# Kernel optimization log

Measured on AMD Instinct MI355X. Metric: run time of the kernel, lower is better.

Reference implementation:

```python
import jax, jax.numpy as jnp
import numpy as np
from jax import lax

KS = 3
PAD = 1
N = KS * KS


def setup_inputs() -> dict:
    key = jax.random.key(0)
    k1, k2, k3, k4, k5, k6 = jax.random.split(key, 6)
    b, cin, cout, h, w = 4, 64, 64, 256, 256
    x = jax.random.normal(k1, (b, cin, h, w), jnp.float32)
    # offset-predicting conv: 2*N output channels, 3x3, pad 1
    p_conv_w = 0.1 * jax.random.normal(k2, (2 * N, cin, KS, KS), jnp.float32)
    p_conv_b = jnp.zeros((2 * N,), jnp.float32)
    # main conv applied to the k*k-expanded sampled map (no bias in original)
    conv_w = jax.random.normal(k3, (cout, cin, KS, KS), jnp.float32) / np.sqrt(cin * N)
    bn_gamma = 1.0 + 0.1 * jax.random.normal(k4, (cout,), jnp.float32)
    bn_beta = 0.1 * jax.random.normal(k5, (cout,), jnp.float32)
    return {"x": x, "p_conv_w": p_conv_w, "p_conv_b": p_conv_b,
            "conv_w": conv_w, "bn_gamma": bn_gamma, "bn_beta": bn_beta}


def _deform_conv(x, p_conv_w, p_conv_b, conv_w, bn_gamma, bn_beta):
    b, c, h, w = x.shape
    # offsets: (b, 2N, h, w) -> (b, h, w, 2N)
    offset = lax.conv_general_dilated(x, p_conv_w, (1, 1), ((PAD, PAD), (PAD, PAD)))
    offset = offset + p_conv_b[None, :, None, None]
    offset = jnp.transpose(offset, (0, 2, 3, 1))
    # zero-pad input; sampling coordinates live on the padded grid
    x_pad = jnp.pad(x, ((0, 0), (0, 0), (PAD, PAD), (PAD, PAD)))
    Hp, Wp = h + 2 * PAD, w + 2 * PAD
    # p = p_0 + p_n + offset  (x/y coords each of shape (b,h,w,N))
    r = jnp.arange(-(KS - 1) // 2, KS // 2 + 1, dtype=jnp.float32)  # [-1,0,1]
    pn_x, pn_y = jnp.meshgrid(r, r, indexing="ij")
    pn_x, pn_y = pn_x.reshape(-1), pn_y.reshape(-1)  # (N,)
    p0_x = jnp.arange(1, h + 1, dtype=jnp.float32)[:, None, None]  # (h,1,1)
    p0_y = jnp.arange(1, w + 1, dtype=jnp.float32)[None, :, None]  # (1,w,1)
    p_x = offset[..., :N] + p0_x + pn_x  # (b,h,w,N)
    p_y = offset[..., N:] + p0_y + pn_y
    # integer corner coords (detached / non-differentiable), clamped
    fx = jnp.floor(lax.stop_gradient(p_x))
    fy = jnp.floor(lax.stop_gradient(p_y))
    q_lt_x = jnp.clip(fx, 0, Hp - 1).astype(jnp.int32)
    q_lt_y = jnp.clip(fy, 0, Wp - 1).astype(jnp.int32)
    q_rb_x = jnp.clip(fx + 1, 0, Hp - 1).astype(jnp.int32)
    q_rb_y = jnp.clip(fy + 1, 0, Wp - 1).astype(jnp.int32)
    # clamped continuous coords (gradient flows to offsets)
    px = jnp.clip(p_x, 0, Hp - 1)
    py = jnp.clip(p_y, 0, Wp - 1)
    # bilinear weights
    ltx = q_lt_x.astype(px.dtype); lty = q_lt_y.astype(px.dtype)
    rbx = q_rb_x.astype(px.dtype); rby = q_rb_y.astype(px.dtype)
    g_lt = (1 + (ltx - px)) * (1 + (lty - py))
    g_rb = (1 - (rbx - px)) * (1 - (rby - py))
    g_lb = (1 + (ltx - px)) * (1 - (rby - py))
    g_rt = (1 - (rbx - px)) * (1 + (lty - py))
    x_flat = x_pad.reshape(b, c, Hp * Wp)

    def gather(qx, qy):
        idx = (qx * Wp + qy).reshape(b, 1, -1)  # (b,1,h*w*N)
        out = jnp.take_along_axis(x_flat, idx, axis=2)
        return out.reshape(b, c, h, w, N)

    x_off = (g_lt[:, None] * gather(q_lt_x, q_lt_y)
             + g_rb[:, None] * gather(q_rb_x, q_rb_y)
             + g_lb[:, None] * gather(q_lt_x, q_rb_y)
             + g_rt[:, None] * gather(q_rb_x, q_lt_y))  # (b,c,h,w,N)
    # conv (kernel=KS, stride=KS on k*k-expanded map) == contraction over (c,N)
    out = jnp.einsum("bchwn,ocn->bohw", x_off, conv_w.reshape(conv_w.shape[0], c, N))
    # BatchNorm2d (training-mode batch statistics) + LeakyReLU(0.1)
    mean = out.mean(axis=(0, 2, 3), keepdims=True)
    var = out.var(axis=(0, 2, 3), keepdims=True)
    y = (out - mean) * lax.rsqrt(var + 1e-5)
    y = y * bn_gamma[None, :, None, None] + bn_beta[None, :, None, None]
    return jnp.where(y > 0, y, 0.1 * y)


def reference(x, p_conv_w, p_conv_b, conv_w, bn_gamma, bn_beta):
    return _deform_conv(x, p_conv_w, p_conv_b, conv_w, bn_gamma, bn_beta)
```

## Files before the change

kernel.cpp:

```cpp
#include <hip/hip_runtime.h>
#include <math.h>

#define BB 4
#define CC 64
#define OCC 64
#define HH 256
#define WW 256
#define HP 258
#define WP 258
#define NPIX (BB * HH * WW)
#define CNT_F 262144.0f

typedef __attribute__((ext_vector_type(8))) __bf16 bf16x8;
typedef __attribute__((ext_vector_type(4))) float f32x4;

__device__ __forceinline__ float blo(unsigned u) {
    return __builtin_bit_cast(float, u << 16);
}
__device__ __forceinline__ float bhi(unsigned u) {
    return __builtin_bit_cast(float, u & 0xffff0000u);
}

__global__ __launch_bounds__(256) void pad_transpose(const float* __restrict__ x,
                                                     __bf16* __restrict__ xt) {
    int blk = blockIdx.x;
    int xchunk = blk & 3;
    int y = (blk >> 2) & 255;
    int b = blk >> 10;
    int tid = threadIdx.x;
    __shared__ float tile[64][65];
    int x0 = xchunk * 64;
    int col = tid & 63;
    int crow = tid >> 6;
    const float* xp = x + ((size_t)b * CC) * HH * WW + (size_t)y * WW + x0;
#pragma unroll
    for (int i = 0; i < 16; ++i) {
        int c = crow + i * 4;
        tile[c][col] = xp[(size_t)c * HH * WW + col];
    }
    __syncthreads();
    __bf16* op = xt + (((size_t)b * HP + (y + 1)) * WP + (x0 + 1)) * CC;
#pragma unroll
    for (int i = 0; i < 16; ++i) {
        int xl = crow + i * 4;
        op[(size_t)xl * CC + col] = (__bf16)tile[col][xl];
    }
}

__global__ void zero_border(__bf16* __restrict__ xt) {
    int i = blockIdx.x * 256 + threadIdx.x;
    const int total = BB * 1028 * CC;
    if (i >= total) return;
    int c = i & 63;
    int p = (i >> 6) % 1028;
    int b = (i >> 6) / 1028;
    int yp, xp;
    if (p < 258)      { yp = 0;           xp = p; }
    else if (p < 516) { yp = 257;         xp = p - 258; }
    else if (p < 772) { yp = p - 516 + 1; xp = 0; }
    else              { yp = p - 772 + 1; xp = 257; }
    xt[(((size_t)b * HP + yp) * WP + xp) * CC + c] = (__bf16)0.0f;
}

__global__ void reorder_weights(const float* __restrict__ cw,
                                const float* __restrict__ pw,
                                __bf16* __restrict__ wtb,
                                __bf16* __restrict__ pwb) {
    int i = blockIdx.x * 256 + threadIdx.x;
    if (i < 36864) {
        int c = i & 63;
        int n = (i >> 6) % 9;
        int oc = i / 576;
        wtb[i] = (__bf16)cw[((size_t)oc * CC + c) * 9 + n];
    } else {
        int j = i - 36864;
        if (j >= 18432) return;
        int c = j & 63;
        int n = (j >> 6) % 9;
        int oc = j / 576;
        pwb[j] = (__bf16)(oc < 18 ? pw[((size_t)oc * CC + c) * 9 + n] : 0.0f);
    }
}

__global__ __launch_bounds__(256, 8) void deform_fused(const __bf16* __restrict__ xt,
                                                       const __bf16* __restrict__ pwb,
                                                       const float* __restrict__ pb,
                                                       const __bf16* __restrict__ wtb,
                                                       float* __restrict__ out) {
    int phys = blockIdx.x;
    int blk = (phys & 7) * 2048 + (phys >> 3);
    int xh = blk & 15;
    int y  = (blk >> 4) & 255;
    int b  = blk >> 12;
    int x0 = xh * 16;
    int tid = threadIdx.x;
    int wave = tid >> 6, lane = tid & 63;
    int chp = lane & 31, half = lane >> 5;

    __shared__ __attribute__((aligned(16))) char smem[19584];
    __bf16 (*sS)[18][72] = (__bf16 (*)[18][72])smem;
    char* sAb = smem;
    float* offbuf = (float*)(smem + 18432);

    {
        const char* base = (const char*)xt + (size_t)b * HP * WP * CC * 2;
        for (int t = tid; t < 1728; t += 256) {
            int pos = t >> 5, cp = t & 31;
            int r = pos / 18, j = pos - r * 18;
            unsigned d = *(const unsigned*)(base
                + (size_t)((y + r) * WP + (x0 + j)) * (CC * 2) + cp * 4);
            *(unsigned*)&sS[r][j][cp * 2] = d;
        }
    }
    __syncthreads();

    if (wave < 2) {
        int nh = wave;
        int m = lane & 15, q = lane >> 4;
        f32x4 acc = {0.0f, 0.0f, 0.0f, 0.0f};
        const __bf16* bp = pwb + (size_t)(nh * 16 + m) * 576 + q * 8;
#pragma unroll
        for (int n = 0; n < 9; ++n) {
            int dy = n / 3, dx = n - dy * 3;
            const __bf16* abase = &sS[dy][m + dx][q * 8];
#pragma unroll
            for (int h = 0; h < 2; ++h) {
                bf16x8 a  = *(const bf16x8*)(abase + h * 32);
                bf16x8 bv = *(const bf16x8*)(bp + n * 64 + h * 32);
                acc = __builtin_amdgcn_mfma_f32_16x16x32_bf16(a, bv, acc, 0, 0, 0);
            }
        }
        int oc = nh * 16 + m;
        if (oc < 18) {
            float bias = pb[oc];
#pragma unroll
            for (int r = 0; r < 4; ++r)
                offbuf[(q * 4 + r) * 18 + oc] = acc[r] + bias;
        }
    }
    __syncthreads();

    float g0 = 0.0f, g1 = 0.0f, g2 = 0.0f, g3 = 0.0f;
    int c0 = 0, c1 = 0, c2 = 0, c3 = 0;
    if (lane < 36) {
        int t = wave * 36 + lane;
        int n = t >> 4, p = t & 15;
        float offx = offbuf[p * 18 + n];
        float offy = offbuf[p * 18 + n + 9];
        float px = offx + (float)(y + 1) + (float)(n / 3 - 1);
        float py = offy + (float)(x0 + p + 1) + (float)(n % 3 - 1);
        float fx = floorf(px), fy = floorf(py);
        float pxc = fminf(fmaxf(px, 0.0f), 257.0f);
        float pyc = fminf(fmaxf(py, 0.0f), 257.0f);
        int ltx = (int)fminf(fmaxf(fx, 0.0f), 257.0f);
        int lty = (int)fminf(fmaxf(fy, 0.0f), 257.0f);
        int rbx = (int)fminf(fmaxf(fx + 1.0f, 0.0f), 257.0f);
        int rby = (int)fminf(fmaxf(fy + 1.0f, 0.0f), 257.0f);
        float dxl = 1.0f + ((float)ltx - pxc);
        float dxr = 1.0f - ((float)rbx - pxc);
        float dyl = 1.0f + ((float)lty - pyc);
        float dyr = 1.0f - ((float)rby - pyc);
        g0 = dxl * dyl;
        g1 = dxr * dyr;
        g2 = dxl * dyr;
        g3 = dxr * dyl;
        c0 = ((ltx * WP + lty) * CC) * 2;
        c1 = ((rbx * WP + rby) * CC) * 2;
        c2 = ((ltx * WP + rby) * CC) * 2;
        c3 = ((rbx * WP + lty) * CC) * 2;
    }

    {
        const char* xbl = (const char*)xt + (size_t)b * HP * WP * CC * 2 + (size_t)chp * 4;
#pragma unroll 3
        for (int r = 0; r < 18; ++r) {
            int src = r * 2 + half;
            float gx = __shfl(g0, src, 64);
            float gy = __shfl(g1, src, 64);
            float gz = __shfl(g2, src, 64);
            float gw = __shfl(g3, src, 64);
            int vx = __shfl(c0, src, 64);
            int vy = __shfl(c1, src, 64);
            int vz = __shfl(c2, src, 64);
            int vw = __shfl(c3, src, 64);
            unsigned d0 = *(const unsigned*)(xbl + vx);
            unsigned d1 = *(const unsigned*)(xbl + vy);
            unsigned d2 = *(const unsigned*)(xbl + vz);
            unsigned d3 = *(const unsigned*)(xbl + vw);
            float lo = gx * blo(d0) + gy * blo(d1) + gz * blo(d2) + gw * blo(d3);
            float hi = gx * bhi(d0) + gy * bhi(d1) + gz * bhi(d2) + gw * bhi(d3);
            __bf16 rlo = (__bf16)lo, rhi = (__bf16)hi;
            ushort2 rv;
            rv.x = __builtin_bit_cast(unsigned short, rlo);
            rv.y = __builtin_bit_cast(unsigned short, rhi);
            int t = wave * 36 + src;
            int n = t >> 4, p = t & 15;
            unsigned bo = (unsigned)p * 1152u + (unsigned)n * 128u + (unsigned)chp * 4u;
            bo ^= (unsigned)((p & 7) << 4);
            *(ushort2*)(sAb + bo) = rv;
        }
    }
    __syncthreads();

    int m = lane & 15, q = lane >> 4;
    f32x4 acc = {0.0f, 0.0f, 0.0f, 0.0f};
    {
        unsigned rowb = (unsigned)m * 1152u;
        unsigned key = (unsigned)((m & 7) << 4);
        const __bf16* bp = wtb + (size_t)(wave * 16 + m) * 576 + q * 8;
        __builtin_amdgcn_s_setprio(1);
#pragma unroll
        for (int k0 = 0; k0 < 576; k0 += 32) {
            unsigned bo = rowb + (((unsigned)(k0 * 2 + q * 16)) ^ key);
            bf16x8 a  = *(const bf16x8*)(sAb + bo);
            bf16x8 bv = *(const bf16x8*)(bp + k0);
            acc = __builtin_amdgcn_mfma_f32_16x16x32_bf16(a, bv, acc, 0, 0, 0);
        }
        __builtin_amdgcn_s_setprio(0);
    }

    int oc = wave * 16 + m;
    float* ob = out + (((size_t)b * OCC + oc) * HH + y) * WW + x0 + q * 4;
    float4 v;
    v.x = acc[0]; v.y = acc[1]; v.z = acc[2]; v.w = acc[3];
    *(float4*)ob = v;
}

__global__ __launch_bounds__(256) void stats_kernel(const float* __restrict__ out,
                                                    float* __restrict__ stats) {
    int blk = blockIdx.x;
    int b = blk & 3;
    int oc = blk >> 2;
    const float* p = out + ((size_t)b * OCC + oc) * HH * WW;
    float s = 0.0f, q = 0.0f;
    for (int i = threadIdx.x; i < HH * WW; i += 256) {
        float v = p[i];
        s += v;
        q += v * v;
    }
#pragma unroll
    for (int d = 1; d < 64; d <<= 1) {
        s += __shfl_xor(s, d, 64);
        q += __shfl_xor(q, d, 64);
    }
    __shared__ float sm[8];
    int wave = threadIdx.x >> 6, lane = threadIdx.x & 63;
    if (lane == 0) { sm[wave] = s; sm[4 + wave] = q; }
    __syncthreads();
    if (threadIdx.x == 0) {
        float ts = sm[0] + sm[1] + sm[2] + sm[3];
        float tq = sm[4] + sm[5] + sm[6] + sm[7];
        atomicAdd(&stats[oc], ts);
        atomicAdd(&stats[64 + oc], tq);
    }
}

__global__ __launch_bounds__(256) void bn_leaky(float* __restrict__ out,
                                                const float* __restrict__ stats,
                                                const float* __restrict__ gamma,
                                                const float* __restrict__ beta) {
    int i = blockIdx.x * 256 + threadIdx.x;
    int oc = (i >> 14) & 63;
    float mean = stats[oc] * (1.0f / CNT_F);
    float var = stats[64 + oc] * (1.0f / CNT_F) - mean * mean;
    float scale = gamma[oc] * rsqrtf(var + 1e-5f);
    float shift = beta[oc] - mean * scale;
    float4* o4 = (float4*)out;
    float4 v = o4[i];
    v.x = v.x * scale + shift; v.x = v.x > 0.0f ? v.x : 0.1f * v.x;
    v.y = v.y * scale + shift; v.y = v.y > 0.0f ? v.y : 0.1f * v.y;
    v.z = v.z * scale + shift; v.z = v.z > 0.0f ? v.z : 0.1f * v.z;
    v.w = v.w * scale + shift; v.w = v.w > 0.0f ? v.w : 0.1f * v.w;
    o4[i] = v;
}

extern "C" void kernel_launch(void* const* d_in, const int* in_sizes, int n_in,
                              void* d_out, int out_size, void* d_ws, size_t ws_size,
                              hipStream_t stream) {
    (void)in_sizes; (void)n_in; (void)out_size; (void)ws_size;
    const float* x     = (const float*)d_in[0];
    const float* pw    = (const float*)d_in[1];
    const float* pb    = (const float*)d_in[2];
    const float* cw    = (const float*)d_in[3];
    const float* gamma = (const float*)d_in[4];
    const float* beta  = (const float*)d_in[5];
    float* out = (float*)d_out;
    char* ws = (char*)d_ws;

    __bf16* xtb  = (__bf16*)ws;
    __bf16* wtb  = (__bf16*)(ws + 34080768 + 18874368);
    __bf16* pwb  = (__bf16*)(ws + 34080768 + 18874368 + 73728);
    float*  stats = (float*)(ws + 34080768 + 18874368 + 73728 + 36864);

    hipMemsetAsync(stats, 0, 128 * sizeof(float), stream);
    pad_transpose<<<4096, 256, 0, stream>>>(x, xtb);
    zero_border<<<(BB * 1028 * CC + 255) / 256, 256, 0, stream>>>(xtb);
    reorder_weights<<<216, 256, 0, stream>>>(cw, pw, wtb, pwb);
    deform_fused<<<16384, 256, 0, stream>>>(xtb, pwb, pb, wtb, out);
    stats_kernel<<<OCC * BB, 256, 0, stream>>>(out, stats);
    bn_leaky<<<NPIX * OCC / 4 / 256, 256, 0, stream>>>(out, stats, gamma, beta);
}
```

Measured before the change: 438.8 us.

## Fuse BN statistics into deform conv epilogue and merge prep kernels

The separate stats pass, which reread the whole 64MB output, is removed. Per-channel sum and sum-of-squares are now reduced inside the deform conv epilogue with wave shuffles and atomics. The pad/transpose, border zeroing, weight reorder and stats memset are merged into a single prep launch to cut launch overhead. The trade-off is many more atomics: two per 16-pixel row segment per channel, landing on 128 addresses, which may contend.

```diff
diff --git a/kernel.cpp b/kernel.cpp
--- a/kernel.cpp
+++ b/kernel.cpp
@@ -21,64 +21,66 @@
     return __builtin_bit_cast(float, u & 0xffff0000u);
 }
 
-__global__ __launch_bounds__(256) void pad_transpose(const float* __restrict__ x,
-                                                     __bf16* __restrict__ xt) {
+__global__ __launch_bounds__(256) void prep(const float* __restrict__ x,
+                                            __bf16* __restrict__ xt,
+                                            const float* __restrict__ cw,
+                                            const float* __restrict__ pw,
+                                            __bf16* __restrict__ wtb,
+                                            __bf16* __restrict__ pwb,
+                                            float* __restrict__ stats) {
     int blk = blockIdx.x;
-    int xchunk = blk & 3;
-    int y = (blk >> 2) & 255;
-    int b = blk >> 10;
     int tid = threadIdx.x;
-    __shared__ float tile[64][65];
-    int x0 = xchunk * 64;
-    int col = tid & 63;
-    int crow = tid >> 6;
-    const float* xp = x + ((size_t)b * CC) * HH * WW + (size_t)y * WW + x0;
-#pragma unroll
-    for (int i = 0; i < 16; ++i) {
-        int c = crow + i * 4;
-        tile[c][col] = xp[(size_t)c * HH * WW + col];
-    }
-    __syncthreads();
-    __bf16* op = xt + (((size_t)b * HP + (y + 1)) * WP + (x0 + 1)) * CC;
-#pragma unroll
-    for (int i = 0; i < 16; ++i) {
-        int xl = crow + i * 4;
-        op[(size_t)xl * CC + col] = (__bf16)tile[col][xl];
-    }
-}
-
-__global__ void zero_border(__bf16* __restrict__ xt) {
-    int i = blockIdx.x * 256 + threadIdx.x;
-    const int total = BB * 1028 * CC;
-    if (i >= total) return;
-    int c = i & 63;
-    int p = (i >> 6) % 1028;
-    int b = (i >> 6) / 1028;
-    int yp, xp;
-    if (p < 258)      { yp = 0;           xp = p; }
-    else if (p < 516) { yp = 257;         xp = p - 258; }
-    else if (p < 772) { yp = p - 516 + 1; xp = 0; }
-    else              { yp = p - 772 + 1; xp = 257; }
-    xt[(((size_t)b * HP + yp) * WP + xp) * CC + c] = (__bf16)0.0f;
-}
-
-__global__ void reorder_weights(const float* __restrict__ cw,
-                                const float* __restrict__ pw,
-                                __bf16* __restrict__ wtb,
-                                __bf16* __restrict__ pwb) {
-    int i = blockIdx.x * 256 + threadIdx.x;
-    if (i < 36864) {
+    if (blk < 4096) {
+        int xchunk = blk & 3;
+        int y = (blk >> 2) & 255;
+        int b = blk >> 10;
+        __shared__ float tile[64][65];
+        int x0 = xchunk * 64;
+        int col = tid & 63;
+        int crow = tid >> 6;
+        const float* xp = x + ((size_t)b * CC) * HH * WW + (size_t)y * WW + x0;
+#pragma unroll
+        for (int i = 0; i < 16; ++i) {
+            int c = crow + i * 4;
+            tile[c][col] = xp[(size_t)c * HH * WW + col];
+        }
+        __syncthreads();
+        __bf16* op = xt + (((size_t)b * HP + (y + 1)) * WP + (x0 + 1)) * CC;
+#pragma unroll
+        for (int i = 0; i < 16; ++i) {
+            int xl = crow + i * 4;
+            op[(size_t)xl * CC + col] = (__bf16)tile[col][xl];
+        }
+    } else if (blk < 5124) {
+        int i = (blk - 4096) * 256 + tid;
+        const int total = BB * 1028 * CC;
+        if (i >= total) return;
         int c = i & 63;
-        int n = (i >> 6) % 9;
-        int oc = i / 576;
-        wtb[i] = (__bf16)cw[((size_t)oc * CC + c) * 9 + n];
+        int p = (i >> 6) % 1028;
+        int b = (i >> 6) / 1028;
+        int yp, xp;
+        if (p < 258)      { yp = 0;           xp = p; }
+        else if (p < 516) { yp = 257;         xp = p - 258; }
+        else if (p < 772) { yp = p - 516 + 1; xp = 0; }
+        else              { yp = p - 772 + 1; xp = 257; }
+        xt[(((size_t)b * HP + yp) * WP + xp) * CC + c] = (__bf16)0.0f;
+    } else if (blk < 5340) {
+        int i = (blk - 5124) * 256 + tid;
+        if (i < 36864) {
+            int c = i & 63;
+            int n = (i >> 6) % 9;
+            int oc = i / 576;
+            wtb[i] = (__bf16)cw[((size_t)oc * CC + c) * 9 + n];
+        } else {
+            int j = i - 36864;
+            if (j >= 18432) return;
+            int c = j & 63;
+            int n = (j >> 6) % 9;
+            int oc = j / 576;
+            pwb[j] = (__bf16)(oc < 18 ? pw[((size_t)oc * CC + c) * 9 + n] : 0.0f);
+        }
     } else {
-        int j = i - 36864;
-        if (j >= 18432) return;
-        int c = j & 63;
-        int n = (j >> 6) % 9;
-        int oc = j / 576;
-        pwb[j] = (__bf16)(oc < 18 ? pw[((size_t)oc * CC + c) * 9 + n] : 0.0f);
+        if (tid < 128) stats[tid] = 0.0f;
     }
 }
 
@@ -86,7 +88,8 @@
                                                        const __bf16* __restrict__ pwb,
                                                        const float* __restrict__ pb,
                                                        const __bf16* __restrict__ wtb,
-                                                       float* __restrict__ out) {
+                                                       float* __restrict__ out,
+                                                       float* __restrict__ stats) {
     int phys = blockIdx.x;
     int blk = (phys & 7) * 2048 + (phys >> 3);
     int xh = blk & 15;
@@ -224,34 +227,19 @@
     float4 v;
     v.x = acc[0]; v.y = acc[1]; v.z = acc[2]; v.w = acc[3];
     *(float4*)ob = v;
-}
-
-__global__ __launch_bounds__(256) void stats_kernel(const float* __restrict__ out,
-                                                    float* __restrict__ stats) {
-    int blk = blockIdx.x;
-    int b = blk & 3;
-    int oc = blk >> 2;
-    const float* p = out + ((size_t)b * OCC + oc) * HH * WW;
-    float s = 0.0f, q = 0.0f;
-    for (int i = threadIdx.x; i < HH * WW; i += 256) {
-        float v = p[i];
-        s += v;
-        q += v * v;
-    }
-#pragma unroll
-    for (int d = 1; d < 64; d <<= 1) {
-        s += __shfl_xor(s, d, 64);
-        q += __shfl_xor(q, d, 64);
-    }
-    __shared__ float sm[8];
-    int wave = threadIdx.x >> 6, lane = threadIdx.x & 63;
-    if (lane == 0) { sm[wave] = s; sm[4 + wave] = q; }
-    __syncthreads();
-    if (threadIdx.x == 0) {
-        float ts = sm[0] + sm[1] + sm[2] + sm[3];
-        float tq = sm[4] + sm[5] + sm[6] + sm[7];
-        atomicAdd(&stats[oc], ts);
-        atomicAdd(&stats[64 + oc], tq);
+
+    {
+        float s  = acc[0] + acc[1] + acc[2] + acc[3];
+        float sq = acc[0] * acc[0] + acc[1] * acc[1]
+                 + acc[2] * acc[2] + acc[3] * acc[3];
+        s  += __shfl_xor(s, 16, 64);
+        sq += __shfl_xor(sq, 16, 64);
+        s  += __shfl_xor(s, 32, 64);
+        sq += __shfl_xor(sq, 32, 64);
+        if (q == 0) {
+            atomicAdd(&stats[oc], s);
+            atomicAdd(&stats[64 + oc], sq);
+        }
     }
 }
 
@@ -292,11 +280,7 @@
     __bf16* pwb  = (__bf16*)(ws + 34080768 + 18874368 + 73728);
     float*  stats = (float*)(ws + 34080768 + 18874368 + 73728 + 36864);
 
-    hipMemsetAsync(stats, 0, 128 * sizeof(float), stream);
-    pad_transpose<<<4096, 256, 0, stream>>>(x, xtb);
-    zero_border<<<(BB * 1028 * CC + 255) / 256, 256, 0, stream>>>(xtb);
-    reorder_weights<<<216, 256, 0, stream>>>(cw, pw, wtb, pwb);
-    deform_fused<<<16384, 256, 0, stream>>>(xtb, pwb, pb, wtb, out);
-    stats_kernel<<<OCC * BB, 256, 0, stream>>>(out, stats);
+    prep<<<5341, 256, 0, stream>>>(x, xtb, cw, pw, wtb, pwb, stats);
+    deform_fused<<<16384, 256, 0, stream>>>(xtb, pwb, pb, wtb, out, stats);
     bn_leaky<<<NPIX * OCC / 4 / 256, 256, 0, stream>>>(out, stats, gamma, beta);
 }
```

Measured after the change: 585.1 us. +33.4%, slower.
